# Performance work log

Measured on AMD Instinct MI355X. Metric: run time of the kernel, lower is better.

The kernel has to match this reference:

```python
import jax, jax.numpy as jnp
import numpy as np

N = 50000
DIM = 768   # input_dim == feature dim (self.L)
D_ATT = 128 # self.D


def setup_inputs() -> dict:
    key = jax.random.key(0)
    ks = jax.random.split(key, 6)
    s = lambda fan_in: 1.0 / np.sqrt(fan_in)
    return {
        "x": jax.random.normal(ks[0], (1, N, DIM), dtype=jnp.float32),
        "W_feat": jax.random.normal(ks[1], (DIM, DIM), dtype=jnp.float32) * s(DIM),
        "b_feat": jax.random.normal(ks[2], (DIM,), dtype=jnp.float32) * s(DIM),
        "W_a": jax.random.normal(ks[3], (D_ATT, DIM), dtype=jnp.float32) * s(DIM),
        "W_b": jax.random.normal(ks[4], (D_ATT, DIM), dtype=jnp.float32) * s(DIM),
        "W_c": jax.random.normal(ks[5], (1, D_ATT), dtype=jnp.float32) * s(D_ATT),
    }


def reference(x, W_feat, b_feat, W_a, W_b, W_c):
    # x: [1, N, DIM] -> squeeze bag dim -> [N, DIM]
    h = jax.nn.relu(jnp.einsum('nd,ed->ne', x[0], W_feat) + b_feat)  # [N, 768]
    a = jax.nn.relu(jnp.einsum('nd,kd->nk', h, W_a))      # [N, 128]
    b = jax.nn.sigmoid(jnp.einsum('nd,kd->nk', h, W_b))   # [N, 128]
    logits = jnp.einsum('nk,ok->on', a * b, W_c)           # [1, N] (transpose fused)
    A = jax.nn.softmax(logits, axis=-1)                    # [1, N]
    return jnp.einsum('on,nd->od', A, h)                   # [1, 768]
```

## Files before the change

### kernel.cpp

```cpp
#include <hip/hip_runtime.h>
#include <hip/hip_bf16.h>
#include <stdint.h>

#define DEVINL __device__ __forceinline__

using bf16x8 = __attribute__((ext_vector_type(8))) short;
using f32x4  = __attribute__((ext_vector_type(4))) float;

static constexpr int NPTS = 50000;
static constexpr int NPAD = 50176;
static constexpr int DIM  = 768;
static constexpr int DATT = 128;
static constexpr int NRB  = NPAD / 128;
static constexpr int NSMB = 49;

DEVINL ushort f2b(float f) {
  uint32_t u = __float_as_uint(f);
  u += 0x7fffu + ((u >> 16) & 1u);
  return (ushort)(u >> 16);
}
DEVINL float b2f(ushort u) { return __uint_as_float(((uint32_t)u) << 16); }

DEVINL void gload_lds16(const void* g, void* l) {
  __builtin_amdgcn_global_load_lds((const __attribute__((address_space(1))) void*)g,
                                   (__attribute__((address_space(3))) void*)l,
                                   16, 0, 0);
}

DEVINL uint32_t cvtpk(float lo, float hi) {
  union { __hip_bfloat162 h2; uint32_t u; } c;
  c.h2 = __float22bfloat162_rn(float2{lo, hi});
  return c.u;
}
DEVINL bf16x8 pack8(f32x4 lo, f32x4 hi) {
  union { uint32_t u[4]; bf16x8 v; } r;
  r.u[0] = cvtpk(lo[0], lo[1]);
  r.u[1] = cvtpk(lo[2], lo[3]);
  r.u[2] = cvtpk(hi[0], hi[1]);
  r.u[3] = cvtpk(hi[2], hi[3]);
  return r.v;
}

__global__ void cvt_weights_kernel(const float* __restrict__ Wf, const float* __restrict__ Wa,
                                   const float* __restrict__ Wb,
                                   ushort* __restrict__ wfb, ushort* __restrict__ wab,
                                   ushort* __restrict__ wbb) {
  const int NF = DIM * DIM / 8, NA = DATT * DIM / 8;
  int i = blockIdx.x * blockDim.x + threadIdx.x;
  const float* src; ushort* dst; int j;
  if (i < NF)               { src = Wf; dst = wfb; j = i; }
  else if (i < NF + NA)     { src = Wa; dst = wab; j = i - NF; }
  else if (i < NF + 2 * NA) { src = Wb; dst = wbb; j = i - NF - NA; }
  else return;
  const float4* s4 = (const float4*)src;
  float4 v0 = s4[(long)j * 2];
  float4 v1 = s4[(long)j * 2 + 1];
  ushort4 o0 = { f2b(v0.x), f2b(v0.y), f2b(v0.z), f2b(v0.w) };
  ushort4 o1 = { f2b(v1.x), f2b(v1.y), f2b(v1.z), f2b(v1.w) };
  ((ushort4*)dst)[(long)j * 2]     = o0;
  ((ushort4*)dst)[(long)j * 2 + 1] = o1;
}

__global__ __launch_bounds__(512, 2)
void gemm_h_fused(const float* __restrict__ X, const ushort* __restrict__ Wfb,
                  const float* __restrict__ bias, ushort* __restrict__ H) {
  __shared__ char lds[2][65536];

  const int tid  = threadIdx.x;
  const int wid  = tid >> 6;
  const int lane = tid & 63;

  const int bid  = blockIdx.x;
  const int wgid = (bid & 7) * 147 + (bid >> 3);
  const int row0 = (wgid / 3) * 128;
  const int col0 = (wgid % 3) * 256;

  const int wrow = (wid >> 2) * 64;
  const int wcol = (wid & 3) * 64;

  f32x4 acc[4][4] = {};

  const int rA   = wid * 4 + (lane >> 4);
  const int swzA = ((lane & 15) ^ (rA & 15)) * 4;
  const int rB   = wid * 8 + (lane >> 3);
  const int swzB = ((lane & 7) ^ (rB & 7)) * 8;

  auto STAGE = [&](int t, int buf) {
    const int k0 = t * 64;
    char* base = &lds[buf][0];
#pragma unroll
    for (int i = 0; i < 4; ++i) {
      const int rg  = row0 + i * 32 + rA;
      const int src = rg < NPTS ? rg : NPTS - 1;
      gload_lds16(X + (long)src * DIM + k0 + swzA, base + (i * 32 + wid * 4) * 256);
    }
#pragma unroll
    for (int i = 0; i < 4; ++i) {
      const int r = i * 64 + rB;
      gload_lds16(Wfb + (long)(col0 + r) * DIM + k0 + swzB,
                  base + 32768 + (i * 64 + wid * 8) * 128);
    }
  };

  auto COMPUTE = [&](int buf) {
    const float*  Ab = (const float*)&lds[buf][0];
    const ushort* Bb = (const ushort*)&lds[buf][32768];
#pragma unroll
    for (int kk = 0; kk < 2; ++kk) {
      const int j = kk * 4 + (lane >> 4);
      bf16x8 a[4];
#pragma unroll
      for (int m = 0; m < 4; ++m) {
        const int ra = wrow + m * 16 + (lane & 15);
        const int s  = ra & 15;
        f32x4 lo = *(const f32x4*)(Ab + ra * 64 + (((2 * j)     ^ s) << 2));
        f32x4 hi = *(const f32x4*)(Ab + ra * 64 + (((2 * j + 1) ^ s) << 2));
        a[m] = pack8(lo, hi);
      }
#pragma unroll
      for (int n = 0; n < 4; ++n) {
        const int rb = wcol + n * 16 + (lane & 15);
        bf16x8 b = *(const bf16x8*)(Bb + rb * 64 + ((j ^ (rb & 7)) << 3));
#pragma unroll
        for (int m = 0; m < 4; ++m)
          acc[m][n] = __builtin_amdgcn_mfma_f32_16x16x32_bf16(a[m], b, acc[m][n], 0, 0, 0);
      }
    }
  };

  STAGE(0, 0);
#pragma unroll 1
  for (int t = 0; t < 12; ++t) {
    if (t < 11) {
      STAGE(t + 1, (t + 1) & 1);
      asm volatile("s_waitcnt vmcnt(8)" ::: "memory");
    } else {
      asm volatile("s_waitcnt vmcnt(0)" ::: "memory");
    }
    __builtin_amdgcn_s_barrier();
    __builtin_amdgcn_sched_barrier(0);
    COMPUTE(t & 1);
    __builtin_amdgcn_sched_barrier(0);
    __builtin_amdgcn_s_barrier();
  }

  const int lq = lane >> 4;
  const int lc = lane & 15;
#pragma unroll
  for (int n = 0; n < 4; ++n) {
    const int cg = col0 + wcol + n * 16 + lc;
    const float bv = bias[cg];
#pragma unroll
    for (int m = 0; m < 4; ++m) {
      const int rg = row0 + wrow + m * 16 + lq * 4;
#pragma unroll
      for (int r2 = 0; r2 < 4; ++r2) {
        float v = acc[m][n][r2] + bv;
        v = fmaxf(v, 0.0f);
        H[(long)(rg + r2) * DIM + cg] = f2b(v);
      }
    }
  }
}

__global__ __launch_bounds__(512)
void gate_kernel(const ushort* __restrict__ Hm, const ushort* __restrict__ Wa,
                 const ushort* __restrict__ Wb, const float* __restrict__ Wc,
                 float* __restrict__ logits) {
  __shared__ ushort Hs [128 * 64];
  __shared__ ushort Was[128 * 64];
  __shared__ ushort Wbs[128 * 64];
  const int tid  = threadIdx.x;
  const int wid  = tid >> 6;
  const int lane = tid & 63;
  const int row0 = blockIdx.x * 128;

  f32x4 fa[8] = {};
  f32x4 fb[8] = {};

  const int ld_r = lane >> 3;
  const int ld_c = (lane & 7) * 8;

  for (int k0 = 0; k0 < DIM; k0 += 64) {
    __syncthreads();
#pragma unroll
    for (int i = 0; i < 2; ++i) {
      const int ch = i * 8 + wid;
      const int r  = ch * 8 + ld_r;
      gload_lds16(Hm + (long)(row0 + r) * DIM + k0 + ld_c, Hs  + ch * 512);
      gload_lds16(Wa + (long)r * DIM        + k0 + ld_c, Was + ch * 512);
      gload_lds16(Wb + (long)r * DIM        + k0 + ld_c, Wbs + ch * 512);
    }
    __syncthreads();
#pragma unroll
    for (int kk = 0; kk < 2; ++kk) {
      const int kc = kk * 32 + (lane >> 4) * 8;
      bf16x8 h = *(const bf16x8*)(Hs + (wid * 16 + (lane & 15)) * 64 + kc);
#pragma unroll
      for (int n = 0; n < 8; ++n) {
        bf16x8 wa = *(const bf16x8*)(Was + (n * 16 + (lane & 15)) * 64 + kc);
        bf16x8 wb = *(const bf16x8*)(Wbs + (n * 16 + (lane & 15)) * 64 + kc);
        fa[n] = __builtin_amdgcn_mfma_f32_16x16x32_bf16(h, wa, fa[n], 0, 0, 0);
        fb[n] = __builtin_amdgcn_mfma_f32_16x16x32_bf16(h, wb, fb[n], 0, 0, 0);
      }
    }
  }

  const int lc = lane & 15;
  const int lq = lane >> 4;
  float g[4];
#pragma unroll
  for (int r = 0; r < 4; ++r) {
    float s = 0.f;
#pragma unroll
    for (int n = 0; n < 8; ++n) {
      float av = fmaxf(fa[n][r], 0.f);
      float sg = 1.f / (1.f + expf(-fb[n][r]));
      s += av * sg * Wc[n * 16 + lc];
    }
    s += __shfl_xor(s, 1);
    s += __shfl_xor(s, 2);
    s += __shfl_xor(s, 4);
    s += __shfl_xor(s, 8);
    g[r] = s;
  }
  if (lc == 0) {
    const int rbase = row0 + wid * 16 + lq * 4;
#pragma unroll
    for (int r = 0; r < 4; ++r) {
      const int nidx = rbase + r;
      if (nidx < NPTS) logits[nidx] = g[r];
    }
  }
}

__global__ __launch_bounds__(1024)
void softmax_part_kernel(const float* __restrict__ logits, float* __restrict__ part2) {
  __shared__ float red[1024];
  const int tid = threadIdx.x;
  const int n = blockIdx.x * 1024 + tid;
  const float v = (n < NPTS) ? logits[n] : -1e30f;
  red[tid] = v; __syncthreads();
  for (int s = 512; s > 0; s >>= 1) {
    if (tid < s) red[tid] = fmaxf(red[tid], red[tid + s]);
    __syncthreads();
  }
  const float m = red[0];
  __syncthreads();
  red[tid] = (n < NPTS) ? expf(v - m) : 0.f;
  __syncthreads();
  for (int s = 512; s > 0; s >>= 1) {
    if (tid < s) red[tid] += red[tid + s];
    __syncthreads();
  }
  if (tid == 0) { part2[blockIdx.x * 2] = m; part2[blockIdx.x * 2 + 1] = red[0]; }
}

__global__ void softmax_comb_kernel(const float* __restrict__ part2,
                                    float* __restrict__ stats) {
  const int l = threadIdx.x;
  float m = (l < NSMB) ? part2[l * 2]     : -1e30f;
  float s = (l < NSMB) ? part2[l * 2 + 1] : 0.f;
  float M = m;
  for (int o = 32; o > 0; o >>= 1) M = fmaxf(M, __shfl_xor(M, o));
  float sc = s * expf(m - M);
  for (int o = 32; o > 0; o >>= 1) sc += __shfl_xor(sc, o);
  if (l == 0) { stats[0] = M; stats[1] = sc; }
}

__global__ __launch_bounds__(192)
void weighted_partial_kernel(const ushort* __restrict__ Hm, const float* __restrict__ logits,
                             const float* __restrict__ stats, float* __restrict__ part) {
  __shared__ float w[128];
  const int b = blockIdx.x, tid = threadIdx.x;
  const int n0 = b * 128;
  if (tid < 128) {
    const int n = n0 + tid;
    w[tid] = (n < NPTS) ? expf(logits[n] - stats[0]) : 0.f;
  }
  __syncthreads();
  float4 acc = {0.f, 0.f, 0.f, 0.f};
  const ushort* hp = Hm + (long)n0 * DIM + tid * 4;
#pragma unroll 4
  for (int r = 0; r < 128; ++r) {
    const float wr = w[r];
    ushort4 v = *(const ushort4*)(hp + (long)r * DIM);
    acc.x += wr * b2f(v.x);
    acc.y += wr * b2f(v.y);
    acc.z += wr * b2f(v.z);
    acc.w += wr * b2f(v.w);
  }
  ((float4*)(part + (long)b * DIM))[tid] = acc;
}

__global__ void final_reduce_kernel(const float* __restrict__ part,
                                    const float* __restrict__ stats,
                                    float* __restrict__ out) {
  const int c = blockIdx.x * blockDim.x + threadIdx.x;
  if (c >= DIM) return;
  float s = 0.f;
  for (int b = 0; b < NRB; ++b) s += part[(long)b * DIM + c];
  out[c] = s / stats[1];
}

extern "C" void kernel_launch(void* const* d_in, const int* in_sizes, int n_in,
                              void* d_out, int out_size, void* d_ws, size_t ws_size,
                              hipStream_t stream) {
  const float* x  = (const float*)d_in[0];
  const float* Wf = (const float*)d_in[1];
  const float* bf = (const float*)d_in[2];
  const float* Wa = (const float*)d_in[3];
  const float* Wb = (const float*)d_in[4];
  const float* Wc = (const float*)d_in[5];
  float* out = (float*)d_out;

  char* p = (char*)d_ws;
  ushort* hb  = (ushort*)p; p += (size_t)NPAD * DIM * 2;
  ushort* wfb = (ushort*)p; p += (size_t)DIM * DIM * 2;
  ushort* wab = (ushort*)p; p += (size_t)DATT * DIM * 2;
  ushort* wbb = (ushort*)p; p += (size_t)DATT * DIM * 2;
  float* logits = (float*)p; p += (size_t)NPAD * 4;
  float* stats  = (float*)p; p += 256;
  float* part2  = (float*)p; p += 1024;
  float* part   = (float*)p; p += (size_t)NRB * DIM * 4;

  cvt_weights_kernel<<<384, 256, 0, stream>>>(Wf, Wa, Wb, wfb, wab, wbb);

  gemm_h_fused<<<392 * 3, 512, 0, stream>>>(x, wfb, bf, hb);
  gate_kernel<<<NRB, 512, 0, stream>>>(hb, wab, wbb, Wc, logits);
  softmax_part_kernel<<<NSMB, 1024, 0, stream>>>(logits, part2);
  softmax_comb_kernel<<<1, 64, 0, stream>>>(part2, stats);
  weighted_partial_kernel<<<NRB, 192, 0, stream>>>(hb, logits, stats, part);
  final_reduce_kernel<<<3, 256, 0, stream>>>(part, stats, out);
}
```

Before: 210.6 us.

## Convert X to bf16 in registers before LDS and triple-buffer the GEMM pipeline

The first GEMM now loads fp32 X tiles into registers, converts them to bf16, and writes them into LDS, instead of DMA-ing fp32 into LDS and converting at every fragment read. This halves the LDS footprint for A and allows a 3-stage buffer with one barrier per iteration. The tile shape changes from 128x256 to 256x128, and MFMA issue is wrapped in setprio. The cost is more registers for the staged A and exposed global-load latency on the register path. The occupancy hint of 2 blocks is also dropped.

```diff
diff --git a/kernel.cpp b/kernel.cpp
--- a/kernel.cpp
+++ b/kernel.cpp
@@ -20,25 +20,16 @@
   return (ushort)(u >> 16);
 }
 DEVINL float b2f(ushort u) { return __uint_as_float(((uint32_t)u) << 16); }
+DEVINL uint32_t cvtpk(float lo, float hi) {
+  union { __hip_bfloat162 h2; uint32_t u; } c;
+  c.h2 = __float22bfloat162_rn(float2{lo, hi});
+  return c.u;
+}
 
 DEVINL void gload_lds16(const void* g, void* l) {
   __builtin_amdgcn_global_load_lds((const __attribute__((address_space(1))) void*)g,
                                    (__attribute__((address_space(3))) void*)l,
                                    16, 0, 0);
-}
-
-DEVINL uint32_t cvtpk(float lo, float hi) {
-  union { __hip_bfloat162 h2; uint32_t u; } c;
-  c.h2 = __float22bfloat162_rn(float2{lo, hi});
-  return c.u;
-}
-DEVINL bf16x8 pack8(f32x4 lo, f32x4 hi) {
-  union { uint32_t u[4]; bf16x8 v; } r;
-  r.u[0] = cvtpk(lo[0], lo[1]);
-  r.u[1] = cvtpk(lo[2], lo[3]);
-  r.u[2] = cvtpk(hi[0], hi[1]);
-  r.u[3] = cvtpk(hi[2], hi[3]);
-  return r.v;
 }
 
 __global__ void cvt_weights_kernel(const float* __restrict__ Wf, const float* __restrict__ Wa,
@@ -61,10 +52,10 @@
   ((ushort4*)dst)[(long)j * 2 + 1] = o1;
 }
 
-__global__ __launch_bounds__(512, 2)
+__global__ __launch_bounds__(512)
 void gemm_h_fused(const float* __restrict__ X, const ushort* __restrict__ Wfb,
                   const float* __restrict__ bias, ushort* __restrict__ H) {
-  __shared__ char lds[2][65536];
+  __shared__ ushort lds[3][24576];
 
   const int tid  = threadIdx.x;
   const int wid  = tid >> 6;
@@ -72,78 +63,108 @@
 
   const int bid  = blockIdx.x;
   const int wgid = (bid & 7) * 147 + (bid >> 3);
-  const int row0 = (wgid / 3) * 128;
-  const int col0 = (wgid % 3) * 256;
-
-  const int wrow = (wid >> 2) * 64;
-  const int wcol = (wid & 3) * 64;
+  const int row0 = (wgid / 6) * 256;
+  const int col0 = (wgid % 6) * 128;
+
+  const int wrow = (wid >> 1) * 64;
+  const int wcol = (wid & 1) * 64;
+
+  const int srow = lane >> 3;
+  const int scol = ((lane & 7) ^ (lane >> 3)) * 8;
+  const ushort* Bbase = Wfb + (long)col0 * DIM;
+  auto STAGE_B = [&](int t, int buf) {
+    const int k0 = t * 64;
+#pragma unroll
+    for (int i = 0; i < 2; ++i) {
+      const int ch = i * 8 + wid;
+      gload_lds16(Bbase + (long)(ch * 8 + srow) * DIM + k0 + scol,
+                  &lds[buf][16384 + ch * 512]);
+    }
+  };
+
+  const int ar  = tid >> 1;
+  const int aj0 = (tid & 1) * 4;
+  const int arow = row0 + ar;
+  const int asrc = arow < NPTS ? arow : NPTS - 1;
+  const float* Abase = X + (long)asrc * DIM + aj0 * 8;
+
+  float4 areg[8];
+  auto LOAD_A = [&](int t) {
+    const float* s = Abase + t * 64;
+#pragma unroll
+    for (int i = 0; i < 8; ++i) areg[i] = *(const float4*)(s + i * 4);
+  };
+  auto WRITE_A = [&](int buf) {
+#pragma unroll
+    for (int w = 0; w < 4; ++w) {
+      const int j = aj0 + w;
+      const int off = ar * 64 + ((j ^ (ar & 7)) << 3);
+      uint4 o;
+      o.x = cvtpk(areg[2 * w].x,     areg[2 * w].y);
+      o.y = cvtpk(areg[2 * w].z,     areg[2 * w].w);
+      o.z = cvtpk(areg[2 * w + 1].x, areg[2 * w + 1].y);
+      o.w = cvtpk(areg[2 * w + 1].z, areg[2 * w + 1].w);
+      *(uint4*)&lds[buf][off] = o;
+    }
+  };
 
   f32x4 acc[4][4] = {};
 
-  const int rA   = wid * 4 + (lane >> 4);
-  const int swzA = ((lane & 15) ^ (rA & 15)) * 4;
-  const int rB   = wid * 8 + (lane >> 3);
-  const int swzB = ((lane & 7) ^ (rB & 7)) * 8;
-
-  auto STAGE = [&](int t, int buf) {
-    const int k0 = t * 64;
-    char* base = &lds[buf][0];
-#pragma unroll
-    for (int i = 0; i < 4; ++i) {
-      const int rg  = row0 + i * 32 + rA;
-      const int src = rg < NPTS ? rg : NPTS - 1;
-      gload_lds16(X + (long)src * DIM + k0 + swzA, base + (i * 32 + wid * 4) * 256);
-    }
-#pragma unroll
-    for (int i = 0; i < 4; ++i) {
-      const int r = i * 64 + rB;
-      gload_lds16(Wfb + (long)(col0 + r) * DIM + k0 + swzB,
-                  base + 32768 + (i * 64 + wid * 8) * 128);
-    }
-  };
-
-  auto COMPUTE = [&](int buf) {
-    const float*  Ab = (const float*)&lds[buf][0];
-    const ushort* Bb = (const ushort*)&lds[buf][32768];
-#pragma unroll
-    for (int kk = 0; kk < 2; ++kk) {
-      const int j = kk * 4 + (lane >> 4);
-      bf16x8 a[4];
-#pragma unroll
-      for (int m = 0; m < 4; ++m) {
-        const int ra = wrow + m * 16 + (lane & 15);
-        const int s  = ra & 15;
-        f32x4 lo = *(const f32x4*)(Ab + ra * 64 + (((2 * j)     ^ s) << 2));
-        f32x4 hi = *(const f32x4*)(Ab + ra * 64 + (((2 * j + 1) ^ s) << 2));
-        a[m] = pack8(lo, hi);
-      }
-#pragma unroll
-      for (int n = 0; n < 4; ++n) {
-        const int rb = wcol + n * 16 + (lane & 15);
-        bf16x8 b = *(const bf16x8*)(Bb + rb * 64 + ((j ^ (rb & 7)) << 3));
-#pragma unroll
-        for (int m = 0; m < 4; ++m)
-          acc[m][n] = __builtin_amdgcn_mfma_f32_16x16x32_bf16(a[m], b, acc[m][n], 0, 0, 0);
-      }
-    }
-  };
-
-  STAGE(0, 0);
+  LOAD_A(0); STAGE_B(0, 0);
+  asm volatile("s_waitcnt vmcnt(2)" ::: "memory");
+  WRITE_A(0);
+  LOAD_A(1); STAGE_B(1, 1);
+  asm volatile("s_waitcnt vmcnt(10)" ::: "memory");
+  asm volatile("s_waitcnt lgkmcnt(0)" ::: "memory");
+  __builtin_amdgcn_s_barrier();
+
 #pragma unroll 1
   for (int t = 0; t < 12; ++t) {
+    const int cb = t % 3;
     if (t < 11) {
-      STAGE(t + 1, (t + 1) & 1);
-      asm volatile("s_waitcnt vmcnt(8)" ::: "memory");
-    } else {
+      asm volatile("s_waitcnt vmcnt(2)" ::: "memory");
+      WRITE_A((t + 1) % 3);
+    }
+    if (t < 10) {
+      LOAD_A(t + 2);
+      STAGE_B(t + 2, (t + 2) % 3);
+    }
+    {
+      const ushort* Ab = &lds[cb][0];
+      const ushort* Bb = &lds[cb][16384];
+#pragma unroll
+      for (int kk = 0; kk < 2; ++kk) {
+        const int j = kk * 4 + (lane >> 4);
+        bf16x8 a[4], b[4];
+#pragma unroll
+        for (int m = 0; m < 4; ++m) {
+          const int ra = wrow + m * 16 + (lane & 15);
+          a[m] = *(const bf16x8*)(Ab + ra * 64 + ((j ^ (ra & 7)) << 3));
+        }
+#pragma unroll
+        for (int n = 0; n < 4; ++n) {
+          const int rb = wcol + n * 16 + (lane & 15);
+          b[n] = *(const bf16x8*)(Bb + rb * 64 + ((j ^ (rb & 7)) << 3));
+        }
+        __builtin_amdgcn_s_setprio(1);
+#pragma unroll
+        for (int n = 0; n < 4; ++n)
+#pragma unroll
+          for (int m = 0; m < 4; ++m)
+            acc[m][n] = __builtin_amdgcn_mfma_f32_16x16x32_bf16(a[m], b[n], acc[m][n], 0, 0, 0);
+        __builtin_amdgcn_s_setprio(0);
+      }
+    }
+    if (t < 10) {
+      asm volatile("s_waitcnt vmcnt(10)" ::: "memory");
+    } else if (t == 10) {
       asm volatile("s_waitcnt vmcnt(0)" ::: "memory");
     }
+    asm volatile("s_waitcnt lgkmcnt(0)" ::: "memory");
     __builtin_amdgcn_s_barrier();
-    __builtin_amdgcn_sched_barrier(0);
-    COMPUTE(t & 1);
-    __builtin_amdgcn_sched_barrier(0);
-    __builtin_amdgcn_s_barrier();
-  }
-
+  }
+
+  __builtin_amdgcn_sched_barrier(0);
   const int lq = lane >> 4;
   const int lc = lane & 15;
 #pragma unroll
@@ -326,7 +347,7 @@
 
   cvt_weights_kernel<<<384, 256, 0, stream>>>(Wf, Wa, Wb, wfb, wab, wbb);
 
-  gemm_h_fused<<<392 * 3, 512, 0, stream>>>(x, wfb, bf, hb);
+  gemm_h_fused<<<196 * 6, 512, 0, stream>>>(x, wfb, bf, hb);
   gate_kernel<<<NRB, 512, 0, stream>>>(hb, wab, wbb, Wc, logits);
   softmax_part_kernel<<<NSMB, 1024, 0, stream>>>(logits, part2);
   softmax_comb_kernel<<<1, 64, 0, stream>>>(part2, stats);
```

Result: slower. 294.4 us (+39.8%).
